# Kernel optimization log

Measured on AMD Instinct MI355X. Metric: run time of the kernel, lower is better.

The kernel has to match this reference:

```python
import jax, jax.numpy as jnp
import numpy as np

NUM, K = 5, 3  # grid intervals and spline order, as in KANLayer(num=5, k=3)

def _grid(num=NUM, k=K, lo=-1.0, hi=1.0):
    # base grid: num+1 points on [lo,hi], extended by k knots on each side (pykan extend_grid)
    h = (hi - lo) / num
    return jnp.linspace(lo - k * h, hi + k * h, num + 1 + 2 * k, dtype=jnp.float32)

def b_spline_basis(x, grid, k=K):
    # Cox-de Boor recursion, identical to pykan B_batch. x: (B, In) -> (B, In, num+k)
    xe = x[..., None]
    b = ((xe >= grid[:-1]) & (xe < grid[1:])).astype(x.dtype)  # order-0 indicators
    for d in range(1, k + 1):
        left = (xe - grid[:-(d + 1)]) / (grid[d:-1] - grid[:-(d + 1)])
        right = (grid[d + 1:] - xe) / (grid[d + 1:] - grid[1:-d])
        b = left * b[..., :-1] + right * b[..., 1:]
    return b

def kan_layer(x, coef, sb, ssp, grid):
    # x: (B, In); coef: (Out, In, nb); sb/ssp: (Out, In). mask == 1.
    basis = b_spline_basis(x, grid)                       # (B, In, nb)
    spline = jnp.einsum('big,oig->boi', basis, coef)      # per-edge spline value
    y = sb[None] * jax.nn.silu(x)[:, None, :] + ssp[None] * spline  # (B, Out, In)
    return y.sum(axis=2)                                  # (B, Out)

def setup_inputs() -> dict:
    key = jax.random.key(0)
    ks = jax.random.split(key, 3)
    B, IN, H, OUT, NB = 128, 3072, 256, 10, NUM + K
    return {
        "x": jax.random.normal(ks[0], (B, IN), jnp.float32),
        "coef1": 0.1 * jax.random.normal(ks[1], (H, IN, NB), jnp.float32),
        "scale_base1": jnp.ones((H, IN), jnp.float32),
        "scale_sp1": jnp.ones((H, IN), jnp.float32),
        "coef2": 0.1 * jax.random.normal(ks[2], (OUT, H, NB), jnp.float32),
        "scale_base2": jnp.ones((OUT, H), jnp.float32),
        "scale_sp2": jnp.ones((OUT, H), jnp.float32),
    }

def reference(x, coef1, scale_base1, scale_sp1, coef2, scale_base2, scale_sp2):
    g = _grid()
    h = kan_layer(x, coef1, scale_base1, scale_sp1, g)
    h = jax.nn.selu(h)
    return kan_layer(h, coef2, scale_base2, scale_sp2, g)
```

## Files before the change

kernel.cpp:

```cpp
#include <hip/hip_runtime.h>
#include <hip/hip_bf16.h>
#include <math.h>


#define B_DIM   128
#define IN1     3072
#define OUT1    256
#define NB      8
#define OUT2    10

#define KTOT    27648
#define ROWB    55296
#define SPLITK  108
#define BN      64

typedef short  bf16x8 __attribute__((ext_vector_type(8)));
typedef float  f32x4  __attribute__((ext_vector_type(4)));
typedef unsigned short ushort_t;
typedef unsigned int u32;

__device__ __forceinline__ ushort_t f2bf(float f) {
    union { __hip_bfloat16 h; ushort_t u; } v;
    v.h = __float2bfloat16(f);
    return v.u;
}

__device__ __forceinline__ void gl_lds16(const void* g, void* l) {
    __builtin_amdgcn_global_load_lds(
        (const __attribute__((address_space(1))) u32*)g,
        (__attribute__((address_space(3))) u32*)l, 16, 0, 0);
}

__device__ __forceinline__ void basis_silu(float x, float w[8], float& sil) {
    sil = x / (1.0f + __expf(-x));
    float u  = (x + 2.2f) * 2.5f;
    float uf = floorf(u);
    int   j  = (int)uf;
    float t  = u - uf;
    float omt = 1.0f - t;
    float t2 = t * t, t3 = t2 * t;
    float w0 = omt * omt * omt * (1.0f / 6.0f);
    float w1 = (3.0f * t3 - 6.0f * t2 + 4.0f) * (1.0f / 6.0f);
    float w2 = (-3.0f * t3 + 3.0f * t2 + 3.0f * t + 1.0f) * (1.0f / 6.0f);
    float w3 = t3 * (1.0f / 6.0f);
    bool valid = (u >= 0.0f) && (u < 11.0f);
#pragma unroll
    for (int g = 0; g < 8; ++g) {
        int m = g - j + 3;
        float v = (m == 0) ? w0 : (m == 1) ? w1 : (m == 2) ? w2 : (m == 3) ? w3 : 0.0f;
        w[g] = valid ? v : 0.0f;
    }
}

__device__ __forceinline__ float selu_f(float x) {
    const float scale = 1.0507009873554805f;
    const float alpha = 1.6732632423543772f;
    return (x > 0.0f) ? scale * x : scale * alpha * (__expf(x) - 1.0f);
}

__global__ __launch_bounds__(128) void kconv(const float* __restrict__ x,
                                             const float* __restrict__ coef1,
                                             const float* __restrict__ sb1,
                                             const float* __restrict__ ssp1,
                                             char* __restrict__ Ag,
                                             char* __restrict__ Wg,
                                             float* __restrict__ h) {
    const int blk = blockIdx.x;
    if (blk < 384) {
        if (blk < 256) h[blk * 128 + threadIdx.x] = 0.0f;

        const int gid = blk * 128 + threadIdx.x;
        const int b  = gid / 384;
        const int ig = gid - b * 384;
        const int i0 = ig * 8;

        float4 x0 = *reinterpret_cast<const float4*>(x + (size_t)b * IN1 + i0);
        float4 x1 = *reinterpret_cast<const float4*>(x + (size_t)b * IN1 + i0 + 4);
        float xa[8] = {x0.x, x0.y, x0.z, x0.w, x1.x, x1.y, x1.z, x1.w};

        float bs[8][8], sil[8];
#pragma unroll
        for (int p = 0; p < 8; ++p) basis_silu(xa[p], bs[p], sil[p]);

        char* rowp = Ag + (size_t)b * ROWB;
        const int qsw = ((ig & 7) ^ (b & 7)) << 4;
#pragma unroll
        for (int s = 0; s < 9; ++s) {
            ushort_t v[8];
#pragma unroll
            for (int p = 0; p < 8; ++p)
                v[p] = f2bf((s < 8) ? bs[p][s] : sil[p]);
            *reinterpret_cast<uint4*>(rowp + (s * 48 + (ig >> 3)) * 128 + qsw) =
                *reinterpret_cast<const uint4*>(v);
        }
    } else {
        const int gid = (blk - 384) * 128 + threadIdx.x;
        const int o  = gid / 384;
        const int ig = gid - o * 384;
        const int i0 = ig * 8;

        float cf[8][8], sspv[8], sbv[8];
#pragma unroll
        for (int p = 0; p < 8; ++p) {
            const float* cp = coef1 + ((size_t)o * IN1 + i0 + p) * NB;
            float4 c0 = *reinterpret_cast<const float4*>(cp);
            float4 c1 = *reinterpret_cast<const float4*>(cp + 4);
            cf[p][0] = c0.x; cf[p][1] = c0.y; cf[p][2] = c0.z; cf[p][3] = c0.w;
            cf[p][4] = c1.x; cf[p][5] = c1.y; cf[p][6] = c1.z; cf[p][7] = c1.w;
        }
        {
            float4 s0 = *reinterpret_cast<const float4*>(ssp1 + (size_t)o * IN1 + i0);
            float4 s1 = *reinterpret_cast<const float4*>(ssp1 + (size_t)o * IN1 + i0 + 4);
            sspv[0]=s0.x; sspv[1]=s0.y; sspv[2]=s0.z; sspv[3]=s0.w;
            sspv[4]=s1.x; sspv[5]=s1.y; sspv[6]=s1.z; sspv[7]=s1.w;
            float4 b0 = *reinterpret_cast<const float4*>(sb1 + (size_t)o * IN1 + i0);
            float4 b1 = *reinterpret_cast<const float4*>(sb1 + (size_t)o * IN1 + i0 + 4);
            sbv[0]=b0.x; sbv[1]=b0.y; sbv[2]=b0.z; sbv[3]=b0.w;
            sbv[4]=b1.x; sbv[5]=b1.y; sbv[6]=b1.z; sbv[7]=b1.w;
        }

        char* rowp = Wg + (size_t)o * ROWB;
        const int qsw = ((ig & 7) ^ (o & 7)) << 4;
#pragma unroll
        for (int s = 0; s < 9; ++s) {
            ushort_t v[8];
#pragma unroll
            for (int p = 0; p < 8; ++p)
                v[p] = f2bf((s < 8) ? cf[p][s] * sspv[p] : sbv[p]);
            *reinterpret_cast<uint4*>(rowp + (s * 48 + (ig >> 3)) * 128 + qsw) =
                *reinterpret_cast<const uint4*>(v);
        }
    }
}

__global__ __launch_bounds__(512) void kgemm(const char* __restrict__ Ag,
                                             const char* __restrict__ Wg,
                                             float* __restrict__ h) {
    __shared__ __align__(16) char lds[2][24576];

    const int tid = threadIdx.x;
    const int w   = tid >> 6, l = tid & 63;
    const int nt  = blockIdx.x, kc = blockIdx.y;
    const int o0  = nt * BN;

    const int ar0 = tid >> 3;
    const int ar1 = 64 + (tid >> 3);
    const int aq  = tid & 7;
    const char* Asrc0 = Ag + (size_t)ar0 * ROWB + ((aq ^ (ar0 & 7)) << 4);
    const char* Asrc1 = Ag + (size_t)ar1 * ROWB + ((aq ^ (ar1 & 7)) << 4);
    const int wr = tid >> 3;
    const char* Wsrc = Wg + (size_t)(o0 + wr) * ROWB + ((aq ^ (wr & 7)) << 4);

#define ISSUE(ss, buf)                                                        \
    {                                                                         \
        const int cb = (kc * 4 + (ss)) * 128;                                 \
        char* base = &lds[buf][0];                                            \
        gl_lds16(Asrc0 + cb, base + w * 1024);                                \
        gl_lds16(Asrc1 + cb, base + 8192 + w * 1024);                         \
        gl_lds16(Wsrc  + cb, base + 16384 + w * 1024);                        \
    }

    f32x4 acc[2][2];
#pragma unroll
    for (int a = 0; a < 2; ++a)
#pragma unroll
        for (int bq = 0; bq < 2; ++bq) acc[a][bq] = (f32x4){0.f, 0.f, 0.f, 0.f};

    const int mq = w >> 1, nq = w & 1;
    const int r16 = l & 15, k16 = l >> 4;

    ISSUE(0, 0)
    ISSUE(1, 1)

#pragma unroll
    for (int s = 0; s < 4; ++s) {
        if (s < 3) { asm volatile("s_waitcnt vmcnt(3)" ::: "memory"); }
        else       { asm volatile("s_waitcnt vmcnt(0)" ::: "memory"); }
        __builtin_amdgcn_s_barrier();
        asm volatile("" ::: "memory");

        const char* Ab = &lds[s & 1][0];
        const char* Wb = &lds[s & 1][16384];
#pragma unroll
        for (int ks = 0; ks < 2; ++ks) {
            const int qf = ks * 4 + k16;
            bf16x8 bf[2], af[2];
#pragma unroll
            for (int bq = 0; bq < 2; ++bq) {
                const int rn = nq * 32 + bq * 16 + r16;
                bf[bq] = *reinterpret_cast<const bf16x8*>(Wb + rn * 128 + ((qf ^ (rn & 7)) << 4));
            }
#pragma unroll
            for (int a = 0; a < 2; ++a) {
                const int rm = mq * 32 + a * 16 + r16;
                af[a] = *reinterpret_cast<const bf16x8*>(Ab + rm * 128 + ((qf ^ (rm & 7)) << 4));
            }
#pragma unroll
            for (int a = 0; a < 2; ++a)
#pragma unroll
                for (int bq = 0; bq < 2; ++bq)
                    acc[a][bq] = __builtin_amdgcn_mfma_f32_16x16x32_bf16(af[a], bf[bq], acc[a][bq], 0, 0, 0);
        }

        __builtin_amdgcn_s_barrier();
        asm volatile("" ::: "memory");
        if (s == 0) ISSUE(2, 0)
        if (s == 1) ISSUE(3, 1)
    }
#undef ISSUE

#pragma unroll
    for (int a = 0; a < 2; ++a) {
#pragma unroll
        for (int bq = 0; bq < 2; ++bq) {
            const int col = o0 + nq * 32 + bq * 16 + r16;
#pragma unroll
            for (int r = 0; r < 4; ++r) {
                const int row = mq * 32 + a * 16 + k16 * 4 + r;
                atomicAdd(&h[(size_t)row * OUT1 + col], acc[a][bq][r]);
            }
        }
    }
}

__global__ __launch_bounds__(256) void klayer2(const float* __restrict__ h,
                                               const float* __restrict__ coef2,
                                               const float* __restrict__ sb2,
                                               const float* __restrict__ ssp2,
                                               float* __restrict__ out) {
    const int b = blockIdx.x;
    const int t = threadIdx.x;
    const float hv = h[b * OUT1 + t];
    const float sh = selu_f(hv);
    float w8[8], sil;
    basis_silu(sh, w8, sil);

    float accs[OUT2];
#pragma unroll
    for (int oo = 0; oo < OUT2; ++oo) {
        const float* cp = coef2 + ((size_t)oo * OUT1 + t) * NB;
        float4 c0 = *reinterpret_cast<const float4*>(cp);
        float4 c1 = *reinterpret_cast<const float4*>(cp + 4);
        float dot = w8[0] * c0.x + w8[1] * c0.y + w8[2] * c0.z + w8[3] * c0.w +
                    w8[4] * c1.x + w8[5] * c1.y + w8[6] * c1.z + w8[7] * c1.w;
        accs[oo] = sb2[oo * OUT1 + t] * sil + ssp2[oo * OUT1 + t] * dot;
    }

    __shared__ float red[4][OUT2];
    const int lane = t & 63, wv = t >> 6;
#pragma unroll
    for (int oo = 0; oo < OUT2; ++oo) {
        float v = accs[oo];
#pragma unroll
        for (int off = 32; off >= 1; off >>= 1) v += __shfl_xor(v, off, 64);
        if (lane == 0) red[wv][oo] = v;
    }
    __syncthreads();
    if (t < OUT2)
        out[b * OUT2 + t] = red[0][t] + red[1][t] + red[2][t] + red[3][t];
}

extern "C" void kernel_launch(void* const* d_in, const int* in_sizes, int n_in,
                              void* d_out, int out_size, void* d_ws, size_t ws_size,
                              hipStream_t stream) {
    const float* x     = (const float*)d_in[0];
    const float* coef1 = (const float*)d_in[1];
    const float* sb1   = (const float*)d_in[2];
    const float* ssp1  = (const float*)d_in[3];
    const float* coef2 = (const float*)d_in[4];
    const float* sb2   = (const float*)d_in[5];
    const float* ssp2  = (const float*)d_in[6];
    float* out = (float*)d_out;

    char*  Ag = (char*)d_ws;
    char*  Wg = Ag + (size_t)B_DIM * ROWB;
    float* h  = (float*)(Wg + (size_t)OUT1 * ROWB);

    kconv<<<1152, 128, 0, stream>>>(x, coef1, sb1, ssp1, Ag, Wg, h);
    kgemm<<<dim3(OUT1 / BN, SPLITK), 512, 0, stream>>>(Ag, Wg, h);
    klayer2<<<B_DIM, 256, 0, stream>>>(h, coef2, sb2, ssp2, out);
}
```

Measured before the change: 43.21 us.

## Replace split-K atomic accumulation with bf16 partial buffers reduced in layer-2 kernel

The GEMM's split-K slices now write per-slice bf16 partial results to a workspace buffer instead of atomically adding fp32 values into h. The layer-2 kernel first sums the 108 partials per output element and then applies SELU and the second KAN layer. This removes atomic contention and the zeroing of h. In exchange it adds a large partial buffer and reads it back, and storing partials in bf16 loses precision in the reduction.

```diff
diff --git a/kernel.cpp b/kernel.cpp
--- a/kernel.cpp
+++ b/kernel.cpp
@@ -23,6 +23,10 @@
     union { __hip_bfloat16 h; ushort_t u; } v;
     v.h = __float2bfloat16(f);
     return v.u;
+}
+__device__ __forceinline__ float bf2f(ushort_t h) {
+    union { float f; u32 u; } v; v.u = ((u32)h) << 16;
+    return v.f;
 }
 
 __device__ __forceinline__ void gl_lds16(const void* g, void* l) {
@@ -63,12 +67,9 @@
                                              const float* __restrict__ sb1,
                                              const float* __restrict__ ssp1,
                                              char* __restrict__ Ag,
-                                             char* __restrict__ Wg,
-                                             float* __restrict__ h) {
+                                             char* __restrict__ Wg) {
     const int blk = blockIdx.x;
     if (blk < 384) {
-        if (blk < 256) h[blk * 128 + threadIdx.x] = 0.0f;
-
         const int gid = blk * 128 + threadIdx.x;
         const int b  = gid / 384;
         const int ig = gid - b * 384;
@@ -135,7 +136,7 @@
 
 __global__ __launch_bounds__(512) void kgemm(const char* __restrict__ Ag,
                                              const char* __restrict__ Wg,
-                                             float* __restrict__ h) {
+                                             ushort_t* __restrict__ partial) {
     __shared__ __align__(16) char lds[2][24576];
 
     const int tid = threadIdx.x;
@@ -209,6 +210,7 @@
     }
 #undef ISSUE
 
+    ushort_t* pp = partial + (size_t)kc * (B_DIM * OUT1);
 #pragma unroll
     for (int a = 0; a < 2; ++a) {
 #pragma unroll
@@ -217,20 +219,35 @@
 #pragma unroll
             for (int r = 0; r < 4; ++r) {
                 const int row = mq * 32 + a * 16 + k16 * 4 + r;
-                atomicAdd(&h[(size_t)row * OUT1 + col], acc[a][bq][r]);
+                pp[(size_t)row * OUT1 + col] = f2bf(acc[a][bq][r]);
             }
         }
     }
 }
 
-__global__ __launch_bounds__(256) void klayer2(const float* __restrict__ h,
-                                               const float* __restrict__ coef2,
-                                               const float* __restrict__ sb2,
-                                               const float* __restrict__ ssp2,
-                                               float* __restrict__ out) {
+__global__ __launch_bounds__(256) void klayer2r(const ushort_t* __restrict__ partial,
+                                                const float* __restrict__ coef2,
+                                                const float* __restrict__ sb2,
+                                                const float* __restrict__ ssp2,
+                                                float* __restrict__ out) {
     const int b = blockIdx.x;
     const int t = threadIdx.x;
-    const float hv = h[b * OUT1 + t];
+    const int w = t >> 6, l = t & 63;
+
+    f32x4 s = {0.f, 0.f, 0.f, 0.f};
+    const ushort_t* pb = partial + (size_t)b * OUT1 + l * 4;
+#pragma unroll
+    for (int c = 0; c < 27; ++c) {
+        ushort4 v = *reinterpret_cast<const ushort4*>(
+            pb + (size_t)(w + 4 * c) * (B_DIM * OUT1));
+        s[0] += bf2f(v.x); s[1] += bf2f(v.y); s[2] += bf2f(v.z); s[3] += bf2f(v.w);
+    }
+
+    __shared__ float sums[4][OUT1];
+    *reinterpret_cast<float4*>(&sums[w][l * 4]) = (float4){s[0], s[1], s[2], s[3]};
+    __syncthreads();
+
+    const float hv = sums[0][t] + sums[1][t] + sums[2][t] + sums[3][t];
     const float sh = selu_f(hv);
     float w8[8], sil;
     basis_silu(sh, w8, sil);
@@ -247,13 +264,12 @@
     }
 
     __shared__ float red[4][OUT2];
-    const int lane = t & 63, wv = t >> 6;
 #pragma unroll
     for (int oo = 0; oo < OUT2; ++oo) {
         float v = accs[oo];
 #pragma unroll
         for (int off = 32; off >= 1; off >>= 1) v += __shfl_xor(v, off, 64);
-        if (lane == 0) red[wv][oo] = v;
+        if (l == 0) red[w][oo] = v;
     }
     __syncthreads();
     if (t < OUT2)
@@ -272,11 +288,11 @@
     const float* ssp2  = (const float*)d_in[6];
     float* out = (float*)d_out;
 
-    char*  Ag = (char*)d_ws;
-    char*  Wg = Ag + (size_t)B_DIM * ROWB;
-    float* h  = (float*)(Wg + (size_t)OUT1 * ROWB);
-
-    kconv<<<1152, 128, 0, stream>>>(x, coef1, sb1, ssp1, Ag, Wg, h);
-    kgemm<<<dim3(OUT1 / BN, SPLITK), 512, 0, stream>>>(Ag, Wg, h);
-    klayer2<<<B_DIM, 256, 0, stream>>>(h, coef2, sb2, ssp2, out);
-}
+    char*     Ag      = (char*)d_ws;
+    char*     Wg      = Ag + (size_t)B_DIM * ROWB;
+    ushort_t* partial = (ushort_t*)(Wg + (size_t)OUT1 * ROWB);
+
+    kconv<<<1152, 128, 0, stream>>>(x, coef1, sb1, ssp1, Ag, Wg);
+    kgemm<<<dim3(OUT1 / BN, SPLITK), 512, 0, stream>>>(Ag, Wg, partial);
+    klayer2r<<<B_DIM, 256, 0, stream>>>(partial, coef2, sb2, ssp2, out);
+}
```

New measurement: 36.27 us. -16.1%, faster.
